# Performance work log

Hardware: AMD Instinct MI355X
Metric: run time of the kernel (lower is better)

## Reference

```python
import jax, jax.numpy as jnp
import numpy as np
import math

DIM = 1024

def setup_inputs() -> dict:
    key = jax.random.key(0)
    ks = jax.random.split(key, 5)
    X = jax.random.normal(ks[0], (4, 2048, DIM), dtype=jnp.float32)
    # Linear params (stored as [in, out] so y = x @ W + b)
    W_in = jax.random.normal(ks[1], (DIM, 3 * DIM), dtype=jnp.float32) / math.sqrt(DIM)
    b_in = jnp.zeros((3 * DIM,), dtype=jnp.float32)
    W_out = jax.random.normal(ks[2], (DIM, DIM), dtype=jnp.float32) / math.sqrt(DIM)
    b_out = jnp.zeros((DIM,), dtype=jnp.float32)
    return {"X": X, "W_in": W_in, "b_in": b_in, "W_out": W_out, "b_out": b_out}

def reference(X, W_in, b_in, W_out, b_out):
    dim = X.shape[-1]
    QKV = X @ W_in + b_in                       # [B, S, 3*dim]
    Q, K, V = jnp.split(QKV, 3, axis=-1)        # each [B, S, dim]
    scores = jnp.einsum('bqd,bkd->bqk', Q, K) / math.sqrt(dim)  # [B, S, S]
    attn = jax.nn.softmax(scores, axis=-1)
    out = jnp.einsum('bqk,bkd->bqd', attn, V)   # [B, S, dim]
    return out @ W_out + b_out
```

## Files before the change

kernel.cpp:

```cpp
#include <hip/hip_runtime.h>
#include <hip/hip_bf16.h>
#include <math.h>

typedef __attribute__((ext_vector_type(8))) __bf16 bf16x8;
typedef __attribute__((ext_vector_type(4))) float f32x4;
typedef __attribute__((ext_vector_type(4))) unsigned int u32x4;

#define DIM 1024
#define SEQ 2048
#define BATCH 4
#define ROWS (BATCH*SEQ)

#define BAR() do { asm volatile("" ::: "memory"); __builtin_amdgcn_s_barrier(); asm volatile("" ::: "memory"); } while(0)
#define WAITV(n) asm volatile("s_waitcnt vmcnt(" #n ")" ::: "memory")
#define WAITL(n) asm volatile("s_waitcnt lgkmcnt(" #n ")" ::: "memory")
#define SCHED0() __builtin_amdgcn_sched_barrier(0)
#define PRIO(x) __builtin_amdgcn_s_setprio(x)

#define DSR(d, a, off) do { u32x4 _t; \
  asm volatile("ds_read_b128 %0, %1 offset:" #off : "=v"(_t) : "v"(a)); \
  (d) = __builtin_bit_cast(bf16x8, _t); } while(0)

__device__ __forceinline__ unsigned short f2bf(float f) {
  unsigned int u = __float_as_uint(f);
  u += 0x7FFF + ((u >> 16) & 1);
  return (unsigned short)(u >> 16);
}
__device__ __forceinline__ unsigned short to_bf_bits(float v) { return f2bf(v); }
__device__ __forceinline__ unsigned short to_bf_bits(unsigned short v) { return v; }

__device__ __forceinline__ void gload_lds16(const void* g, void* lds) {
  __builtin_amdgcn_global_load_lds((__attribute__((address_space(1))) void*)g,
                                   (__attribute__((address_space(3))) void*)lds,
                                   16, 0, 0);
}

__global__ __launch_bounds__(256)
void conv_f32_bf16(const float* __restrict__ src, unsigned short* __restrict__ dst, int n8) {
  int i = blockIdx.x * blockDim.x + threadIdx.x;
  if (i >= n8) return;
  const float4* s = reinterpret_cast<const float4*>(src) + (size_t)i * 2;
  float4 a = s[0], b = s[1];
  union { unsigned short h[8]; uint4 v; } p;
  p.h[0]=f2bf(a.x); p.h[1]=f2bf(a.y); p.h[2]=f2bf(a.z); p.h[3]=f2bf(a.w);
  p.h[4]=f2bf(b.x); p.h[5]=f2bf(b.y); p.h[6]=f2bf(b.z); p.h[7]=f2bf(b.w);
  reinterpret_cast<uint4*>(dst)[i] = p.v;
}

template<typename Tin>
__global__ __launch_bounds__(1024)
void transpose_conv(const Tin* __restrict__ src, int ldsrc, size_t sstride,
                    unsigned short* __restrict__ dst, int lddst, size_t dstride) {
  __shared__ unsigned short tile[32][33];
  const Tin* s = src + (size_t)blockIdx.z * sstride;
  unsigned short* d = dst + (size_t)blockIdx.z * dstride;
  int tx = threadIdx.x, ty = threadIdx.y;
  int r = blockIdx.y * 32 + ty, c = blockIdx.x * 32 + tx;
  tile[ty][tx] = to_bf_bits(s[(size_t)r * ldsrc + c]);
  __syncthreads();
  d[(size_t)(blockIdx.x * 32 + ty) * lddst + blockIdx.y * 32 + tx] = tile[tx][ty];
}

#define EPI_QKV 0
#define EPI_F32 1
#define EPI_BF16 2
#define EPI_BIAS_F32 3

template<int BN, int EPI>
__global__ __launch_bounds__(512, 2)
void gemm8(const unsigned short* __restrict__ A, int lda, size_t sA,
           const unsigned short* __restrict__ B, int ldb, size_t sB,
           void* __restrict__ C, int ldc, size_t sC,
           const float* __restrict__ bias, int K) {
  constexpr int NREP = BN / 64;
  constexpr int NW = 16 * NREP;
  __shared__ unsigned short As[2 * 256 * 64];
  __shared__ unsigned short Bs[2 * BN * 64];

  const int tid = threadIdx.x;
  const int lane = tid & 63, wave = tid >> 6;
  const int wm = wave >> 2, wn = wave & 3;
  const int fr = lane & 15, fk = lane >> 4;
  const int tileM = blockIdx.y * 256, tileN = blockIdx.x * BN;
  const unsigned short* Ab = A + (size_t)blockIdx.z * sA;
  const unsigned short* Bb = B + (size_t)blockIdx.z * sB;

  const int srow = tid >> 3;
  const int sg = (tid & 7) ^ (srow & 7);

  auto stageA = [&](int buf, int half, int k0) {
#pragma unroll
    for (int q = 0; q < 2; ++q) {
      int rl = half * 128 + q * 64 + srow;
      gload_lds16(Ab + (size_t)(tileM + rl) * lda + k0 + sg * 8,
                  &As[buf * (256 * 64) + rl * 64 + (tid & 7) * 8]);
    }
  };
  auto stageB = [&](int buf, int half, int k0) {
#pragma unroll
    for (int q = 0; q < 2; ++q) {
      int rl = half * 128 + q * 64 + srow;
      gload_lds16(Bb + (size_t)(tileN + rl) * ldb + k0 + sg * 8,
                  &Bs[buf * (BN * 64) + rl * 64 + (tid & 7) * 8]);
    }
  };

  f32x4 acc[8][NREP];
#pragma unroll
  for (int m = 0; m < 8; ++m)
#pragma unroll
    for (int n = 0; n < NREP; ++n) acc[m][n] = (f32x4){0.f, 0.f, 0.f, 0.f};

  const int NS = K >> 6;
  const unsigned asb = (unsigned)(size_t)(__attribute__((address_space(3))) unsigned short*)As;
  const unsigned bsb = (unsigned)(size_t)(__attribute__((address_space(3))) unsigned short*)Bs;
  const unsigned aoff = (unsigned)((wm * 128 + fr) * 128 + ((fk ^ (fr & 7)) << 4));
  const unsigned boff = (unsigned)((wn * NW + fr) * 128 + ((fk ^ (fr & 7)) << 4));
  auto aBase = [&](int b) { return asb + (unsigned)b * 32768u + aoff; };
  auto bBase = [&](int b) { return bsb + (unsigned)b * (unsigned)(BN * 128) + boff; };

  if constexpr (BN == 256) {
    bf16x8 afLo[4][2], afHi[4][2], bgA[2][2], bgB[2][2];
    stageB(0, 0, 0); stageB(0, 1, 0); stageA(0, 0, 0); stageA(0, 1, 0);
    if (NS > 1) { stageB(1, 0, 64); stageB(1, 1, 64); WAITV(4); } else { WAITV(0); }
    BAR();
    {
      unsigned a0 = aBase(0), a1 = a0 ^ 64u, b0 = bBase(0), b1 = b0 ^ 64u;
      DSR(afLo[0][0], a0, 0); DSR(afLo[1][0], a0, 2048); DSR(afLo[2][0], a0, 4096); DSR(afLo[3][0], a0, 6144);
      DSR(afLo[0][1], a1, 0); DSR(afLo[1][1], a1, 2048); DSR(afLo[2][1], a1, 4096); DSR(afLo[3][1], a1, 6144);
      DSR(bgA[0][0], b0, 0); DSR(bgA[1][0], b0, 2048);
      DSR(bgA[0][1], b1, 0); DSR(bgA[1][1], b1, 2048);
    }
    for (int t = 0; t < NS; ++t) {
      const int cb = t & 1, nb = cb ^ 1;
      const unsigned cA0 = aBase(cb), cA1 = cA0 ^ 64u, cB0 = bBase(cb), cB1 = cB0 ^ 64u;
      const unsigned nA0 = aBase(nb), nA1 = nA0 ^ 64u, nB0 = bBase(nb), nB1 = nB0 ^ 64u;
      const int k1 = (t + 1) << 6, k2 = (t + 2) << 6;
      DSR(bgB[0][0], cB0, 4096); DSR(bgB[1][0], cB0, 6144);
      DSR(bgB[0][1], cB1, 4096); DSR(bgB[1][1], cB1, 6144);
      if (t + 1 < NS) stageA(nb, 0, k1);
      BAR(); WAITL(4); SCHED0();
      PRIO(1);
#pragma unroll
      for (int kk = 0; kk < 2; ++kk)
#pragma unroll
        for (int m = 0; m < 4; ++m)
#pragma unroll
          for (int n = 0; n < 2; ++n)
            acc[m][n] = __builtin_amdgcn_mfma_f32_16x16x32_bf16(afLo[m][kk], bgA[n][kk], acc[m][n], 0, 0, 0);
      PRIO(0); SCHED0();
      BAR();
      DSR(afHi[0][0], cA0, 8192); DSR(afHi[1][0], cA0, 10240); DSR(afHi[2][0], cA0, 12288); DSR(afHi[3][0], cA0, 14336);
      DSR(afHi[0][1], cA1, 8192); DSR(afHi[1][1], cA1, 10240); DSR(afHi[2][1], cA1, 12288); DSR(afHi[3][1], cA1, 14336);
      if (t + 1 < NS) stageA(nb, 1, k1);
      if (t + 2 < NS) stageB(cb, 0, k2);
      BAR(); WAITL(8); SCHED0();
      PRIO(1);
#pragma unroll
      for (int kk = 0; kk < 2; ++kk)
#pragma unroll
        for (int m = 0; m < 4; ++m)
#pragma unroll
          for (int n = 0; n < 2; ++n)
            acc[m][2 + n] = __builtin_amdgcn_mfma_f32_16x16x32_bf16(afLo[m][kk], bgB[n][kk], acc[m][2 + n], 0, 0, 0);
      PRIO(0); SCHED0();
      BAR();
      if (t + 2 < NS) stageB(cb, 1, k2);
      BAR(); WAITL(0); SCHED0();
      PRIO(1);
#pragma unroll
      for (int kk = 0; kk < 2; ++kk)
#pragma unroll
        for (int m = 0; m < 4; ++m)
#pragma unroll
          for (int n = 0; n < 2; ++n)
            acc[4 + m][n] = __builtin_amdgcn_mfma_f32_16x16x32_bf16(afHi[m][kk], bgA[n][kk], acc[4 + m][n], 0, 0, 0);
      PRIO(0); SCHED0();
      if (t + 1 < NS) { if (t + 2 < NS) { WAITV(4); } else { WAITV(0); } }
      BAR();
      if (t + 1 < NS) {
        DSR(afLo[0][0], nA0, 0); DSR(afLo[1][0], nA0, 2048); DSR(afLo[2][0], nA0, 4096); DSR(afLo[3][0], nA0, 6144);
        DSR(afLo[0][1], nA1, 0); DSR(afLo[1][1], nA1, 2048); DSR(afLo[2][1], nA1, 4096); DSR(afLo[3][1], nA1, 6144);
        DSR(bgA[0][0], nB0, 0); DSR(bgA[1][0], nB0, 2048);
        DSR(bgA[0][1], nB1, 0); DSR(bgA[1][1], nB1, 2048);
      }
      SCHED0();
      PRIO(1);
#pragma unroll
      for (int kk = 0; kk < 2; ++kk)
#pragma unroll
        for (int m = 0; m < 4; ++m)
#pragma unroll
          for (int n = 0; n < 2; ++n)
            acc[4 + m][2 + n] = __builtin_amdgcn_mfma_f32_16x16x32_bf16(afHi[m][kk], bgB[n][kk], acc[4 + m][2 + n], 0, 0, 0);
      PRIO(0); SCHED0();
      BAR();
    }
  } else {
    bf16x8 a0f[4], a1f[4], h0f[4], h1f[4], b0f[2], b1f[2];
    stageB(0, 0, 0); stageA(0, 0, 0); stageA(0, 1, 0);
    if (NS > 1) { stageB(1, 0, 64); WAITV(2); } else { WAITV(0); }
    BAR();
    {
      unsigned a0 = aBase(0), b0 = bBase(0);
      DSR(a0f[0], a0, 0); DSR(a0f[1], a0, 2048); DSR(a0f[2], a0, 4096); DSR(a0f[3], a0, 6144);
      DSR(b0f[0], b0, 0); DSR(b0f[1], b0, 2048);
    }
    for (int t = 0; t < NS; ++t) {
      const int cb = t & 1, nb = cb ^ 1;
      const unsigned cA0 = aBase(cb), cA1 = cA0 ^ 64u, cB0 = bBase(cb), cB1 = cB0 ^ 64u;
      const unsigned nA0 = aBase(nb), nB0 = bBase(nb);
      const int k1 = (t + 1) << 6, k2 = (t + 2) << 6;
      DSR(a1f[0], cA1, 0); DSR(a1f[1], cA1, 2048); DSR(a1f[2], cA1, 4096); DSR(a1f[3], cA1, 6144);
      DSR(b1f[0], cB1, 0); DSR(b1f[1], cB1, 2048);
      if (t + 1 < NS) stageA(nb, 0, k1);
      BAR(); WAITL(6); SCHED0();
      PRIO(1);
#pragma unroll
      for (int m = 0; m < 4; ++m)
#pragma unroll
        for (int n = 0; n < 2; ++n)
          acc[m][n] = __builtin_amdgcn_mfma_f32_16x16x32_bf16(a0f[m], b0f[n], acc[m][n], 0, 0, 0);
      PRIO(0); SCHED0();
      BAR();
      DSR(h0f[0], cA0, 8192); DSR(h0f[1], cA0, 10240); DSR(h0f[2], cA0, 12288); DSR(h0f[3], cA0, 14336);
      if (t + 1 < NS) stageA(nb, 1, k1);
      BAR(); WAITL(4); SCHED0();
      PRIO(1);
#pragma unroll
      for (int m = 0; m < 4; ++m)
#pragma unroll
        for (int n = 0; n < 2; ++n)
          acc[m][n] = __builtin_amdgcn_mfma_f32_16x16x32_bf16(a1f[m], b1f[n], acc[m][n], 0, 0, 0);
      PRIO(0); SCHED0();
      BAR();
      DSR(h1f[0], cA1, 8192); DSR(h1f[1], cA1, 10240); DSR(h1f[2], cA1, 12288); DSR(h1f[3], cA1, 14336);
      if (t + 2 < NS) stageB(cb, 0, k2);
      BAR(); WAITL(4); SCHED0();
      PRIO(1);
#pragma unroll
      for (int m = 0; m < 4; ++m)
#pragma unroll
        for (int n = 0; n < 2; ++n)
          acc[4 + m][n] = __builtin_amdgcn_mfma_f32_16x16x32_bf16(h0f[m], b0f[n], acc[4 + m][n], 0, 0, 0);
      PRIO(0); SCHED0();
      if (t + 1 < NS) { if (t + 2 < NS) { WAITV(2); } else { WAITV(0); } }
      BAR();
      if (t + 1 < NS) {
        DSR(a0f[0], nA0, 0); DSR(a0f[1], nA0, 2048); DSR(a0f[2], nA0, 4096); DSR(a0f[3], nA0, 6144);
        DSR(b0f[0], nB0, 0); DSR(b0f[1], nB0, 2048);
        WAITL(6);
      } else {
        WAITL(0);
      }
      SCHED0();
      PRIO(1);
#pragma unroll
      for (int m = 0; m < 4; ++m)
#pragma unroll
        for (int n = 0; n < 2; ++n)
          acc[4 + m][n] = __builtin_amdgcn_mfma_f32_16x16x32_bf16(h1f[m], b1f[n], acc[4 + m][n], 0, 0, 0);
      PRIO(0); SCHED0();
      BAR();
    }
  }

#pragma unroll
  for (int m = 0; m < 8; ++m)
#pragma unroll
    for (int n = 0; n < NREP; ++n)
#pragma unroll
      for (int j = 0; j < 4; ++j) {
        int row = tileM + wm * 128 + m * 16 + fk * 4 + j;
        int col = tileN + wn * NW + n * 16 + fr;
        float v = acc[m][n][j];
        if (EPI == EPI_QKV) {
          v += bias[col];
          if (col < DIM) v *= 0.03125f;
          ((unsigned short*)C + (size_t)blockIdx.z * sC)[(size_t)row * ldc + col] = f2bf(v);
        } else if (EPI == EPI_BF16) {
          ((unsigned short*)C + (size_t)blockIdx.z * sC)[(size_t)row * ldc + col] = f2bf(v);
        } else if (EPI == EPI_BIAS_F32) {
          ((float*)C + (size_t)blockIdx.z * sC)[(size_t)row * ldc + col] = v + bias[col];
        } else {
          ((float*)C + (size_t)blockIdx.z * sC)[(size_t)row * ldc + col] = v;
        }
      }
}

__global__ __launch_bounds__(256)
void softmax_kernel(float* __restrict__ S, size_t zstride) {
  __shared__ float red[8];
  float* row = S + (size_t)blockIdx.y * zstride + (size_t)blockIdx.x * SEQ;
  const int tid = threadIdx.x;
  const int lane = tid & 63, wave = tid >> 6;
  const float4* src = reinterpret_cast<const float4*>(row) + tid * 2;
  float4 a = src[0], b = src[1];
  float v[8] = {a.x, a.y, a.z, a.w, b.x, b.y, b.z, b.w};
  float m = v[0];
#pragma unroll
  for (int i = 1; i < 8; ++i) m = fmaxf(m, v[i]);
  for (int o = 32; o; o >>= 1) m = fmaxf(m, __shfl_xor(m, o));
  if (lane == 0) red[wave] = m;
  __syncthreads();
  m = fmaxf(fmaxf(red[0], red[1]), fmaxf(red[2], red[3]));
  float e[8], s = 0.f;
#pragma unroll
  for (int i = 0; i < 8; ++i) { e[i] = expf(v[i] - m); s += e[i]; }
  for (int o = 32; o; o >>= 1) s += __shfl_xor(s, o);
  if (lane == 0) red[4 + wave] = s;
  __syncthreads();
  s = red[4] + red[5] + red[6] + red[7];
  float inv = 1.f / s;
  union { unsigned short h[8]; uint4 u; } p;
#pragma unroll
  for (int i = 0; i < 8; ++i) p.h[i] = f2bf(e[i] * inv);
  reinterpret_cast<uint4*>(row)[tid] = p.u;
}

extern "C" void kernel_launch(void* const* d_in, const int* in_sizes, int n_in,
                              void* d_out, int out_size, void* d_ws, size_t ws_size,
                              hipStream_t stream) {
  const float* X     = (const float*)d_in[0];
  const float* W_in  = (const float*)d_in[1];
  const float* b_in  = (const float*)d_in[2];
  const float* W_out = (const float*)d_in[3];
  const float* b_out = (const float*)d_in[4];
  float* out = (float*)d_out;
  char* ws = (char*)d_ws;

  size_t o = 0;
  auto alloc = [&](size_t bytes) { size_t r = o; o += (bytes + 255) & ~(size_t)255; return r; };
  unsigned short* Xbf   = (unsigned short*)(ws + alloc((size_t)ROWS * DIM * 2));
  unsigned short* WinT  = (unsigned short*)(ws + alloc((size_t)3 * DIM * DIM * 2));
  unsigned short* WoutT = (unsigned short*)(ws + alloc((size_t)DIM * DIM * 2));
  unsigned short* QKV   = (unsigned short*)(ws + alloc((size_t)ROWS * 3 * DIM * 2));
  size_t fixed = o;
  size_t per_batch = (((size_t)SEQ * SEQ * 4 + 255) & ~(size_t)255) +
                     (((size_t)DIM * SEQ * 2 + 255) & ~(size_t)255);
  int G = (ws_size >= fixed + 4 * per_batch) ? BATCH : 1;
  float*          Sc = (float*)(ws + alloc((size_t)G * SEQ * SEQ * 4));
  unsigned short* Vt = (unsigned short*)(ws + alloc((size_t)G * DIM * SEQ * 2));
  unsigned short* O  = Xbf;

  conv_f32_bf16<<<(ROWS * DIM / 8 + 255) / 256, 256, 0, stream>>>(X, Xbf, ROWS * DIM / 8);
  transpose_conv<float><<<dim3(3 * DIM / 32, DIM / 32, 1), dim3(32, 32), 0, stream>>>(
      W_in, 3 * DIM, 0, WinT, DIM, 0);
  transpose_conv<float><<<dim3(DIM / 32, DIM / 32, 1), dim3(32, 32), 0, stream>>>(
      W_out, DIM, 0, WoutT, DIM, 0);
  gemm8<128, EPI_QKV><<<dim3(3 * DIM / 128, ROWS / 256, 1), 512, 0, stream>>>(
      Xbf, DIM, 0, WinT, DIM, 0, QKV, 3 * DIM, 0, b_in, DIM);

  for (int b0 = 0; b0 < BATCH; b0 += G) {
    const unsigned short* Qb = QKV + (size_t)b0 * SEQ * 3 * DIM;
    const unsigned short* Kb = Qb + DIM;
    const unsigned short* Vb = Qb + 2 * DIM;
    transpose_conv<unsigned short><<<dim3(DIM / 32, SEQ / 32, G), dim3(32, 32), 0, stream>>>(
        Vb, 3 * DIM, (size_t)SEQ * 3 * DIM, Vt, SEQ, (size_t)DIM * SEQ);
    gemm8<256, EPI_F32><<<dim3(SEQ / 256, SEQ / 256, G), 512, 0, stream>>>(
        Qb, 3 * DIM, (size_t)SEQ * 3 * DIM, Kb, 3 * DIM, (size_t)SEQ * 3 * DIM,
        Sc, SEQ, (size_t)SEQ * SEQ, nullptr, DIM);
    softmax_kernel<<<dim3(SEQ, G), 256, 0, stream>>>(Sc, (size_t)SEQ * SEQ);
    gemm8<128, EPI_BF16><<<dim3(DIM / 128, SEQ / 256, G), 512, 0, stream>>>(
        (const unsigned short*)Sc, 2 * SEQ, (size_t)2 * SEQ * SEQ,
        Vt, SEQ, (size_t)DIM * SEQ,
        O + (size_t)b0 * SEQ * DIM, DIM, (size_t)SEQ * DIM, nullptr, SEQ);
  }
  gemm8<128, EPI_BIAS_F32><<<dim3(DIM / 128, ROWS / 256, 1), 512, 0, stream>>>(
      O, DIM, 0, WoutT, DIM, 0, out, DIM, 0, b_out, DIM);
}
```

Before: 228.5 us.

## Fuse softmax into PV GEMM and add triple-buffered BN128 GEMM kernel

Removes the separate softmax pass. A new pv_fused kernel computes row max and sum with an online reduction over the fp32 scores. It then exponentiates, normalizes and converts score tiles to bf16 while staging them into LDS for the P·V MFMA loop, with a 3-deep ring buffer for V. The QKV and output projections move to a new gemm1b kernel with a simpler triple-buffered pipeline. The fused kernel reads the fp32 score matrix twice (stats pass plus operand pass) and recomputes exp inside the GEMM, in exchange for dropping the softmax write and reread.

```diff
diff --git a/kernel.cpp b/kernel.cpp
--- a/kernel.cpp
+++ b/kernel.cpp
@@ -20,6 +20,8 @@
 #define DSR(d, a, off) do { u32x4 _t; \
   asm volatile("ds_read_b128 %0, %1 offset:" #off : "=v"(_t) : "v"(a)); \
   (d) = __builtin_bit_cast(bf16x8, _t); } while(0)
+#define GLD4(d, p, off) asm volatile("global_load_dwordx4 %0, %1, off offset:" #off \
+  : "=&v"(d) : "v"(p))
 
 __device__ __forceinline__ unsigned short f2bf(float f) {
   unsigned int u = __float_as_uint(f);
@@ -66,17 +68,15 @@
 #define EPI_BF16 2
 #define EPI_BIAS_F32 3
 
-template<int BN, int EPI>
+template<int EPI>
 __global__ __launch_bounds__(512, 2)
 void gemm8(const unsigned short* __restrict__ A, int lda, size_t sA,
            const unsigned short* __restrict__ B, int ldb, size_t sB,
            void* __restrict__ C, int ldc, size_t sC,
            const float* __restrict__ bias, int K) {
-  constexpr int NREP = BN / 64;
-  constexpr int NW = 16 * NREP;
+  constexpr int BN = 256, NREP = 4, NW = 64;
   __shared__ unsigned short As[2 * 256 * 64];
   __shared__ unsigned short Bs[2 * BN * 64];
-
   const int tid = threadIdx.x;
   const int lane = tid & 63, wave = tid >> 6;
   const int wm = wave >> 2, wn = wave & 3;
@@ -84,7 +84,6 @@
   const int tileM = blockIdx.y * 256, tileN = blockIdx.x * BN;
   const unsigned short* Ab = A + (size_t)blockIdx.z * sA;
   const unsigned short* Bb = B + (size_t)blockIdx.z * sB;
-
   const int srow = tid >> 3;
   const int sg = (tid & 7) ^ (srow & 7);
 
@@ -119,150 +118,81 @@
   auto aBase = [&](int b) { return asb + (unsigned)b * 32768u + aoff; };
   auto bBase = [&](int b) { return bsb + (unsigned)b * (unsigned)(BN * 128) + boff; };
 
-  if constexpr (BN == 256) {
-    bf16x8 afLo[4][2], afHi[4][2], bgA[2][2], bgB[2][2];
-    stageB(0, 0, 0); stageB(0, 1, 0); stageA(0, 0, 0); stageA(0, 1, 0);
-    if (NS > 1) { stageB(1, 0, 64); stageB(1, 1, 64); WAITV(4); } else { WAITV(0); }
+  bf16x8 afLo[4][2], afHi[4][2], bgA[2][2], bgB[2][2];
+  stageB(0, 0, 0); stageB(0, 1, 0); stageA(0, 0, 0); stageA(0, 1, 0);
+  if (NS > 1) { stageB(1, 0, 64); stageB(1, 1, 64); WAITV(4); } else { WAITV(0); }
+  BAR();
+  {
+    unsigned a0 = aBase(0), a1 = a0 ^ 64u, b0 = bBase(0), b1 = b0 ^ 64u;
+    DSR(afLo[0][0], a0, 0); DSR(afLo[1][0], a0, 2048); DSR(afLo[2][0], a0, 4096); DSR(afLo[3][0], a0, 6144);
+    DSR(afLo[0][1], a1, 0); DSR(afLo[1][1], a1, 2048); DSR(afLo[2][1], a1, 4096); DSR(afLo[3][1], a1, 6144);
+    DSR(bgA[0][0], b0, 0); DSR(bgA[1][0], b0, 2048);
+    DSR(bgA[0][1], b1, 0); DSR(bgA[1][1], b1, 2048);
+  }
+  for (int t = 0; t < NS; ++t) {
+    const int cb = t & 1, nb = cb ^ 1;
+    const unsigned cA0 = aBase(cb), cA1 = cA0 ^ 64u, cB0 = bBase(cb), cB1 = cB0 ^ 64u;
+    const unsigned nA0 = aBase(nb), nA1 = nA0 ^ 64u, nB0 = bBase(nb), nB1 = nB0 ^ 64u;
+    const int k1 = (t + 1) << 6, k2 = (t + 2) << 6;
+    DSR(bgB[0][0], cB0, 4096); DSR(bgB[1][0], cB0, 6144);
+    DSR(bgB[0][1], cB1, 4096); DSR(bgB[1][1], cB1, 6144);
+    if (t + 1 < NS) stageA(nb, 0, k1);
+    BAR(); WAITL(4); SCHED0();
+    PRIO(1);
+#pragma unroll
+    for (int kk = 0; kk < 2; ++kk)
+#pragma unroll
+      for (int m = 0; m < 4; ++m)
+#pragma unroll
+        for (int n = 0; n < 2; ++n)
+          acc[m][n] = __builtin_amdgcn_mfma_f32_16x16x32_bf16(afLo[m][kk], bgA[n][kk], acc[m][n], 0, 0, 0);
+    PRIO(0); SCHED0();
     BAR();
-    {
-      unsigned a0 = aBase(0), a1 = a0 ^ 64u, b0 = bBase(0), b1 = b0 ^ 64u;
-      DSR(afLo[0][0], a0, 0); DSR(afLo[1][0], a0, 2048); DSR(afLo[2][0], a0, 4096); DSR(afLo[3][0], a0, 6144);
-      DSR(afLo[0][1], a1, 0); DSR(afLo[1][1], a1, 2048); DSR(afLo[2][1], a1, 4096); DSR(afLo[3][1], a1, 6144);
-      DSR(bgA[0][0], b0, 0); DSR(bgA[1][0], b0, 2048);
-      DSR(bgA[0][1], b1, 0); DSR(bgA[1][1], b1, 2048);
-    }
-    for (int t = 0; t < NS; ++t) {
-      const int cb = t & 1, nb = cb ^ 1;
-      const unsigned cA0 = aBase(cb), cA1 = cA0 ^ 64u, cB0 = bBase(cb), cB1 = cB0 ^ 64u;
-      const unsigned nA0 = aBase(nb), nA1 = nA0 ^ 64u, nB0 = bBase(nb), nB1 = nB0 ^ 64u;
-      const int k1 = (t + 1) << 6, k2 = (t + 2) << 6;
-      DSR(bgB[0][0], cB0, 4096); DSR(bgB[1][0], cB0, 6144);
-      DSR(bgB[0][1], cB1, 4096); DSR(bgB[1][1], cB1, 6144);
-      if (t + 1 < NS) stageA(nb, 0, k1);
-      BAR(); WAITL(4); SCHED0();
-      PRIO(1);
-#pragma unroll
-      for (int kk = 0; kk < 2; ++kk)
-#pragma unroll
-        for (int m = 0; m < 4; ++m)
-#pragma unroll
-          for (int n = 0; n < 2; ++n)
-            acc[m][n] = __builtin_amdgcn_mfma_f32_16x16x32_bf16(afLo[m][kk], bgA[n][kk], acc[m][n], 0, 0, 0);
-      PRIO(0); SCHED0();
-      BAR();
-      DSR(afHi[0][0], cA0, 8192); DSR(afHi[1][0], cA0, 10240); DSR(afHi[2][0], cA0, 12288); DSR(afHi[3][0], cA0, 14336);
-      DSR(afHi[0][1], cA1, 8192); DSR(afHi[1][1], cA1, 10240); DSR(afHi[2][1], cA1, 12288); DSR(afHi[3][1], cA1, 14336);
-      if (t + 1 < NS) stageA(nb, 1, k1);
-      if (t + 2 < NS) stageB(cb, 0, k2);
-      BAR(); WAITL(8); SCHED0();
-      PRIO(1);
-#pragma unroll
-      for (int kk = 0; kk < 2; ++kk)
-#pragma unroll
-        for (int m = 0; m < 4; ++m)
-#pragma unroll
-          for (int n = 0; n < 2; ++n)
-            acc[m][2 + n] = __builtin_amdgcn_mfma_f32_16x16x32_bf16(afLo[m][kk], bgB[n][kk], acc[m][2 + n], 0, 0, 0);
-      PRIO(0); SCHED0();
-      BAR();
-      if (t + 2 < NS) stageB(cb, 1, k2);
-      BAR(); WAITL(0); SCHED0();
-      PRIO(1);
-#pragma unroll
-      for (int kk = 0; kk < 2; ++kk)
-#pragma unroll
-        for (int m = 0; m < 4; ++m)
-#pragma unroll
-          for (int n = 0; n < 2; ++n)
-            acc[4 + m][n] = __builtin_amdgcn_mfma_f32_16x16x32_bf16(afHi[m][kk], bgA[n][kk], acc[4 + m][n], 0, 0, 0);
-      PRIO(0); SCHED0();
-      if (t + 1 < NS) { if (t + 2 < NS) { WAITV(4); } else { WAITV(0); } }
-      BAR();
-      if (t + 1 < NS) {
-        DSR(afLo[0][0], nA0, 0); DSR(afLo[1][0], nA0, 2048); DSR(afLo[2][0], nA0, 4096); DSR(afLo[3][0], nA0, 6144);
-        DSR(afLo[0][1], nA1, 0); DSR(afLo[1][1], nA1, 2048); DSR(afLo[2][1], nA1, 4096); DSR(afLo[3][1], nA1, 6144);
-        DSR(bgA[0][0], nB0, 0); DSR(bgA[1][0], nB0, 2048);
-        DSR(bgA[0][1], nB1, 0); DSR(bgA[1][1], nB1, 2048);
-      }
-      SCHED0();
-      PRIO(1);
-#pragma unroll
-      for (int kk = 0; kk < 2; ++kk)
-#pragma unroll
-        for (int m = 0; m < 4; ++m)
-#pragma unroll
-          for (int n = 0; n < 2; ++n)
-            acc[4 + m][2 + n] = __builtin_amdgcn_mfma_f32_16x16x32_bf16(afHi[m][kk], bgB[n][kk], acc[4 + m][2 + n], 0, 0, 0);
-      PRIO(0); SCHED0();
-      BAR();
-    }
-  } else {
-    bf16x8 a0f[4], a1f[4], h0f[4], h1f[4], b0f[2], b1f[2];
-    stageB(0, 0, 0); stageA(0, 0, 0); stageA(0, 1, 0);
-    if (NS > 1) { stageB(1, 0, 64); WAITV(2); } else { WAITV(0); }
+    DSR(afHi[0][0], cA0, 8192); DSR(afHi[1][0], cA0, 10240); DSR(afHi[2][0], cA0, 12288); DSR(afHi[3][0], cA0, 14336);
+    DSR(afHi[0][1], cA1, 8192); DSR(afHi[1][1], cA1, 10240); DSR(afHi[2][1], cA1, 12288); DSR(afHi[3][1], cA1, 14336);
+    if (t + 1 < NS) stageA(nb, 1, k1);
+    if (t + 2 < NS) stageB(cb, 0, k2);
+    BAR(); WAITL(8); SCHED0();
+    PRIO(1);
+#pragma unroll
+    for (int kk = 0; kk < 2; ++kk)
+#pragma unroll
+      for (int m = 0; m < 4; ++m)
+#pragma unroll
+        for (int n = 0; n < 2; ++n)
+          acc[m][2 + n] = __builtin_amdgcn_mfma_f32_16x16x32_bf16(afLo[m][kk], bgB[n][kk], acc[m][2 + n], 0, 0, 0);
+    PRIO(0); SCHED0();
     BAR();
-    {
-      unsigned a0 = aBase(0), b0 = bBase(0);
-      DSR(a0f[0], a0, 0); DSR(a0f[1], a0, 2048); DSR(a0f[2], a0, 4096); DSR(a0f[3], a0, 6144);
-      DSR(b0f[0], b0, 0); DSR(b0f[1], b0, 2048);
-    }
-    for (int t = 0; t < NS; ++t) {
-      const int cb = t & 1, nb = cb ^ 1;
-      const unsigned cA0 = aBase(cb), cA1 = cA0 ^ 64u, cB0 = bBase(cb), cB1 = cB0 ^ 64u;
-      const unsigned nA0 = aBase(nb), nB0 = bBase(nb);
-      const int k1 = (t + 1) << 6, k2 = (t + 2) << 6;
-      DSR(a1f[0], cA1, 0); DSR(a1f[1], cA1, 2048); DSR(a1f[2], cA1, 4096); DSR(a1f[3], cA1, 6144);
-      DSR(b1f[0], cB1, 0); DSR(b1f[1], cB1, 2048);
-      if (t + 1 < NS) stageA(nb, 0, k1);
-      BAR(); WAITL(6); SCHED0();
-      PRIO(1);
-#pragma unroll
-      for (int m = 0; m < 4; ++m)
-#pragma unroll
-        for (int n = 0; n < 2; ++n)
-          acc[m][n] = __builtin_amdgcn_mfma_f32_16x16x32_bf16(a0f[m], b0f[n], acc[m][n], 0, 0, 0);
-      PRIO(0); SCHED0();
-      BAR();
-      DSR(h0f[0], cA0, 8192); DSR(h0f[1], cA0, 10240); DSR(h0f[2], cA0, 12288); DSR(h0f[3], cA0, 14336);
-      if (t + 1 < NS) stageA(nb, 1, k1);
-      BAR(); WAITL(4); SCHED0();
-      PRIO(1);
-#pragma unroll
-      for (int m = 0; m < 4; ++m)
-#pragma unroll
-        for (int n = 0; n < 2; ++n)
-          acc[m][n] = __builtin_amdgcn_mfma_f32_16x16x32_bf16(a1f[m], b1f[n], acc[m][n], 0, 0, 0);
-      PRIO(0); SCHED0();
-      BAR();
-      DSR(h1f[0], cA1, 8192); DSR(h1f[1], cA1, 10240); DSR(h1f[2], cA1, 12288); DSR(h1f[3], cA1, 14336);
-      if (t + 2 < NS) stageB(cb, 0, k2);
-      BAR(); WAITL(4); SCHED0();
-      PRIO(1);
-#pragma unroll
-      for (int m = 0; m < 4; ++m)
-#pragma unroll
-        for (int n = 0; n < 2; ++n)
-          acc[4 + m][n] = __builtin_amdgcn_mfma_f32_16x16x32_bf16(h0f[m], b0f[n], acc[4 + m][n], 0, 0, 0);
-      PRIO(0); SCHED0();
-      if (t + 1 < NS) { if (t + 2 < NS) { WAITV(2); } else { WAITV(0); } }
-      BAR();
-      if (t + 1 < NS) {
-        DSR(a0f[0], nA0, 0); DSR(a0f[1], nA0, 2048); DSR(a0f[2], nA0, 4096); DSR(a0f[3], nA0, 6144);
-        DSR(b0f[0], nB0, 0); DSR(b0f[1], nB0, 2048);
-        WAITL(6);
-      } else {
-        WAITL(0);
-      }
-      SCHED0();
-      PRIO(1);
-#pragma unroll
-      for (int m = 0; m < 4; ++m)
-#pragma unroll
-        for (int n = 0; n < 2; ++n)
-          acc[4 + m][n] = __builtin_amdgcn_mfma_f32_16x16x32_bf16(h1f[m], b1f[n], acc[4 + m][n], 0, 0, 0);
-      PRIO(0); SCHED0();
-      BAR();
-    }
+    if (t + 2 < NS) stageB(cb, 1, k2);
+    BAR(); WAITL(0); SCHED0();
+    PRIO(1);
+#pragma unroll
+    for (int kk = 0; kk < 2; ++kk)
+#pragma unroll
+      for (int m = 0; m < 4; ++m)
+#pragma unroll
+        for (int n = 0; n < 2; ++n)
+          acc[4 + m][n] = __builtin_amdgcn_mfma_f32_16x16x32_bf16(afHi[m][kk], bgA[n][kk], acc[4 + m][n], 0, 0, 0);
+    PRIO(0); SCHED0();
+    if (t + 1 < NS) { if (t + 2 < NS) { WAITV(4); } else { WAITV(0); } }
+    BAR();
+    if (t + 1 < NS) {
+      DSR(afLo[0][0], nA0, 0); DSR(afLo[1][0], nA0, 2048); DSR(afLo[2][0], nA0, 4096); DSR(afLo[3][0], nA0, 6144);
+      DSR(afLo[0][1], nA1, 0); DSR(afLo[1][1], nA1, 2048); DSR(afLo[2][1], nA1, 4096); DSR(afLo[3][1], nA1, 6144);
+      DSR(bgA[0][0], nB0, 0); DSR(bgA[1][0], nB0, 2048);
+      DSR(bgA[0][1], nB1, 0); DSR(bgA[1][1], nB1, 2048);
+    }
+    SCHED0();
+    PRIO(1);
+#pragma unroll
+    for (int kk = 0; kk < 2; ++kk)
+#pragma unroll
+      for (int m = 0; m < 4; ++m)
+#pragma unroll
+        for (int n = 0; n < 2; ++n)
+          acc[4 + m][2 + n] = __builtin_amdgcn_mfma_f32_16x16x32_bf16(afHi[m][kk], bgB[n][kk], acc[4 + m][2 + n], 0, 0, 0);
+    PRIO(0); SCHED0();
+    BAR();
   }
 
 #pragma unroll
@@ -274,48 +204,257 @@
         int row = tileM + wm * 128 + m * 16 + fk * 4 + j;
         int col = tileN + wn * NW + n * 16 + fr;
         float v = acc[m][n][j];
+        if (EPI == EPI_F32) {
+          ((float*)C + (size_t)blockIdx.z * sC)[(size_t)row * ldc + col] = v;
+        } else {
+          ((float*)C + (size_t)blockIdx.z * sC)[(size_t)row * ldc + col] = v + bias[col];
+        }
+      }
+}
+
+template<int EPI>
+__global__ __launch_bounds__(512, 2)
+void gemm1b(const unsigned short* __restrict__ A, int lda,
+            const unsigned short* __restrict__ B, int ldb,
+            void* __restrict__ C, int ldc,
+            const float* __restrict__ bias, int K) {
+  __shared__ unsigned short As[3 * 256 * 64];
+  __shared__ unsigned short Bs[3 * 128 * 64];
+  const int tid = threadIdx.x;
+  const int lane = tid & 63, wave = tid >> 6;
+  const int wm = wave >> 2, wn = wave & 3;
+  const int fr = lane & 15, fk = lane >> 4;
+  const int tileM = blockIdx.y * 256, tileN = blockIdx.x * 128;
+  const int srow = tid >> 3;
+
+  auto stageT = [&](int ring, int k0) {
+#pragma unroll
+    for (int q = 0; q < 4; ++q) {
+      int rl = q * 64 + srow;
+      int sg = (tid & 7) ^ (rl & 7);
+      gload_lds16(A + (size_t)(tileM + rl) * lda + k0 + sg * 8,
+                  &As[ring * (256 * 64) + rl * 64 + (tid & 7) * 8]);
+    }
+#pragma unroll
+    for (int q = 0; q < 2; ++q) {
+      int rl = q * 64 + srow;
+      int sg = (tid & 7) ^ (rl & 7);
+      gload_lds16(B + (size_t)(tileN + rl) * ldb + k0 + sg * 8,
+                  &Bs[ring * (128 * 64) + rl * 64 + (tid & 7) * 8]);
+    }
+  };
+
+  f32x4 acc[8][2];
+#pragma unroll
+  for (int m = 0; m < 8; ++m)
+#pragma unroll
+    for (int n = 0; n < 2; ++n) acc[m][n] = (f32x4){0.f, 0.f, 0.f, 0.f};
+
+  const int NS = K >> 6;
+  const unsigned asb = (unsigned)(size_t)(__attribute__((address_space(3))) unsigned short*)As;
+  const unsigned bsb = (unsigned)(size_t)(__attribute__((address_space(3))) unsigned short*)Bs;
+  const unsigned aoff = (unsigned)((wm * 128 + fr) * 128 + ((fk ^ (fr & 7)) << 4));
+  const unsigned boff = (unsigned)((wn * 32 + fr) * 128 + ((fk ^ (fr & 7)) << 4));
+
+  stageT(0, 0); stageT(1, 64);
+  WAITV(6); BAR();
+
+  bf16x8 afLo[4][2], afHi[4][2], bg[2][2];
+  int ring = 0;
+  for (int t = 0; t < NS; ++t) {
+    const unsigned aT0 = asb + (unsigned)ring * 32768u + aoff, aT1 = aT0 ^ 64u;
+    const unsigned bT0 = bsb + (unsigned)ring * 16384u + boff, bT1 = bT0 ^ 64u;
+    if (t + 2 < NS) stageT((t + 2) % 3, (t + 2) << 6);
+    DSR(afLo[0][0], aT0, 0); DSR(afLo[1][0], aT0, 2048); DSR(afLo[2][0], aT0, 4096); DSR(afLo[3][0], aT0, 6144);
+    DSR(afLo[0][1], aT1, 0); DSR(afLo[1][1], aT1, 2048); DSR(afLo[2][1], aT1, 4096); DSR(afLo[3][1], aT1, 6144);
+    DSR(bg[0][0], bT0, 0); DSR(bg[1][0], bT0, 2048);
+    DSR(bg[0][1], bT1, 0); DSR(bg[1][1], bT1, 2048);
+    WAITL(0); SCHED0();
+    PRIO(1);
+#pragma unroll
+    for (int kk = 0; kk < 2; ++kk)
+#pragma unroll
+      for (int m = 0; m < 4; ++m)
+#pragma unroll
+        for (int n = 0; n < 2; ++n)
+          acc[m][n] = __builtin_amdgcn_mfma_f32_16x16x32_bf16(afLo[m][kk], bg[n][kk], acc[m][n], 0, 0, 0);
+    PRIO(0); SCHED0();
+    DSR(afHi[0][0], aT0, 8192); DSR(afHi[1][0], aT0, 10240); DSR(afHi[2][0], aT0, 12288); DSR(afHi[3][0], aT0, 14336);
+    DSR(afHi[0][1], aT1, 8192); DSR(afHi[1][1], aT1, 10240); DSR(afHi[2][1], aT1, 12288); DSR(afHi[3][1], aT1, 14336);
+    WAITL(0); SCHED0();
+    PRIO(1);
+#pragma unroll
+    for (int kk = 0; kk < 2; ++kk)
+#pragma unroll
+      for (int m = 0; m < 4; ++m)
+#pragma unroll
+        for (int n = 0; n < 2; ++n)
+          acc[4 + m][n] = __builtin_amdgcn_mfma_f32_16x16x32_bf16(afHi[m][kk], bg[n][kk], acc[4 + m][n], 0, 0, 0);
+    PRIO(0); SCHED0();
+    if (t + 1 < NS) { if (t + 2 < NS) { WAITV(6); } else { WAITV(0); } }
+    BAR();
+    ring = (ring + 1) % 3;
+  }
+
+#pragma unroll
+  for (int m = 0; m < 8; ++m)
+#pragma unroll
+    for (int n = 0; n < 2; ++n)
+#pragma unroll
+      for (int j = 0; j < 4; ++j) {
+        int row = tileM + wm * 128 + m * 16 + fk * 4 + j;
+        int col = tileN + wn * 32 + n * 16 + fr;
+        float v = acc[m][n][j];
         if (EPI == EPI_QKV) {
           v += bias[col];
           if (col < DIM) v *= 0.03125f;
-          ((unsigned short*)C + (size_t)blockIdx.z * sC)[(size_t)row * ldc + col] = f2bf(v);
-        } else if (EPI == EPI_BF16) {
-          ((unsigned short*)C + (size_t)blockIdx.z * sC)[(size_t)row * ldc + col] = f2bf(v);
+          ((unsigned short*)C)[(size_t)row * ldc + col] = f2bf(v);
         } else if (EPI == EPI_BIAS_F32) {
-          ((float*)C + (size_t)blockIdx.z * sC)[(size_t)row * ldc + col] = v + bias[col];
+          ((float*)C)[(size_t)row * ldc + col] = v + bias[col];
         } else {
-          ((float*)C + (size_t)blockIdx.z * sC)[(size_t)row * ldc + col] = v;
+          ((unsigned short*)C)[(size_t)row * ldc + col] = f2bf(v);
         }
       }
 }
 
-__global__ __launch_bounds__(256)
-void softmax_kernel(float* __restrict__ S, size_t zstride) {
-  __shared__ float red[8];
-  float* row = S + (size_t)blockIdx.y * zstride + (size_t)blockIdx.x * SEQ;
+__global__ __launch_bounds__(512, 2)
+void pv_fused(const float* __restrict__ S, size_t sS,
+              const unsigned short* __restrict__ Vt, size_t sV,
+              unsigned short* __restrict__ O, size_t sO) {
+  __shared__ unsigned short As[2 * 128 * 64];
+  __shared__ unsigned short Bs[3 * 256 * 64];
+  __shared__ float mrow[128], ilrow[128];
   const int tid = threadIdx.x;
   const int lane = tid & 63, wave = tid >> 6;
-  const float4* src = reinterpret_cast<const float4*>(row) + tid * 2;
-  float4 a = src[0], b = src[1];
-  float v[8] = {a.x, a.y, a.z, a.w, b.x, b.y, b.z, b.w};
-  float m = v[0];
-#pragma unroll
-  for (int i = 1; i < 8; ++i) m = fmaxf(m, v[i]);
-  for (int o = 32; o; o >>= 1) m = fmaxf(m, __shfl_xor(m, o));
-  if (lane == 0) red[wave] = m;
+  const int wm = wave >> 2, wn = wave & 3;
+  const int fr = lane & 15, fk = lane >> 4;
+  const int tileM = blockIdx.y * 128, tileN = blockIdx.x * 256;
+  const float* Sb = S + (size_t)blockIdx.z * sS;
+  const unsigned short* Vb = Vt + (size_t)blockIdx.z * sV;
+
+  {
+    int r = tid >> 2, q = tid & 3;
+    const float4* rowp = (const float4*)(Sb + (size_t)(tileM + r) * SEQ);
+    float m = -3.4e38f, l = 0.f;
+    for (int i = q; i < SEQ / 4; i += 4) {
+      float4 v = rowp[i];
+      float mx = fmaxf(fmaxf(v.x, v.y), fmaxf(v.z, v.w));
+      if (mx > m) { l *= __expf(m - mx); m = mx; }
+      l += __expf(v.x - m) + __expf(v.y - m) + __expf(v.z - m) + __expf(v.w - m);
+    }
+#pragma unroll
+    for (int o = 1; o < 4; o <<= 1) {
+      float mo = __shfl_xor(m, o), lo = __shfl_xor(l, o);
+      float mn = fmaxf(m, mo);
+      l = l * __expf(m - mn) + lo * __expf(mo - mn); m = mn;
+    }
+    if (q == 0) { mrow[r] = m; ilrow[r] = 1.f / l; }
+  }
   __syncthreads();
-  m = fmaxf(fmaxf(red[0], red[1]), fmaxf(red[2], red[3]));
-  float e[8], s = 0.f;
-#pragma unroll
-  for (int i = 0; i < 8; ++i) { e[i] = expf(v[i] - m); s += e[i]; }
-  for (int o = 32; o; o >>= 1) s += __shfl_xor(s, o);
-  if (lane == 0) red[4 + wave] = s;
-  __syncthreads();
-  s = red[4] + red[5] + red[6] + red[7];
-  float inv = 1.f / s;
-  union { unsigned short h[8]; uint4 u; } p;
-#pragma unroll
-  for (int i = 0; i < 8; ++i) p.h[i] = f2bf(e[i] * inv);
-  reinterpret_cast<uint4*>(row)[tid] = p.u;
+
+  const int sr = tid >> 2;
+  const float mr = mrow[sr], ilr = ilrow[sr];
+  const int scol = (tid & 3) * 16;
+  const int s0 = (tid & 3) * 2;
+  const int p0 = s0 ^ (sr & 7), p1 = (s0 + 1) ^ (sr & 7);
+  const int srow = tid >> 3;
+
+  auto stageB = [&](int ring, int k0) {
+#pragma unroll
+    for (int q = 0; q < 4; ++q) {
+      int rl = q * 64 + srow;
+      int sg = (tid & 7) ^ (rl & 7);
+      gload_lds16(Vb + (size_t)(tileN + rl) * SEQ + k0 + sg * 8,
+                  &Bs[ring * (256 * 64) + rl * 64 + (tid & 7) * 8]);
+    }
+  };
+  float4 st0, st1, st2, st3;
+  auto issueA = [&](int k0) {
+    const float* ap = Sb + (size_t)(tileM + sr) * SEQ + k0 + scol;
+    GLD4(st0, ap, 0); GLD4(st1, ap, 16); GLD4(st2, ap, 32); GLD4(st3, ap, 48);
+  };
+  auto writeA = [&](int buf) {
+    union { unsigned short h[8]; uint4 u; } a, b;
+    a.h[0]=f2bf(__expf(st0.x-mr)*ilr); a.h[1]=f2bf(__expf(st0.y-mr)*ilr);
+    a.h[2]=f2bf(__expf(st0.z-mr)*ilr); a.h[3]=f2bf(__expf(st0.w-mr)*ilr);
+    a.h[4]=f2bf(__expf(st1.x-mr)*ilr); a.h[5]=f2bf(__expf(st1.y-mr)*ilr);
+    a.h[6]=f2bf(__expf(st1.z-mr)*ilr); a.h[7]=f2bf(__expf(st1.w-mr)*ilr);
+    b.h[0]=f2bf(__expf(st2.x-mr)*ilr); b.h[1]=f2bf(__expf(st2.y-mr)*ilr);
+    b.h[2]=f2bf(__expf(st2.z-mr)*ilr); b.h[3]=f2bf(__expf(st2.w-mr)*ilr);
+    b.h[4]=f2bf(__expf(st3.x-mr)*ilr); b.h[5]=f2bf(__expf(st3.y-mr)*ilr);
+    b.h[6]=f2bf(__expf(st3.z-mr)*ilr); b.h[7]=f2bf(__expf(st3.w-mr)*ilr);
+    *(uint4*)&As[buf * (128 * 64) + sr * 64 + p0 * 8] = a.u;
+    *(uint4*)&As[buf * (128 * 64) + sr * 64 + p1 * 8] = b.u;
+  };
+
+  f32x4 acc[4][4];
+#pragma unroll
+  for (int m = 0; m < 4; ++m)
+#pragma unroll
+    for (int n = 0; n < 4; ++n) acc[m][n] = (f32x4){0.f, 0.f, 0.f, 0.f};
+
+  const int NS = SEQ >> 6;
+  const unsigned asb = (unsigned)(size_t)(__attribute__((address_space(3))) unsigned short*)As;
+  const unsigned bsb = (unsigned)(size_t)(__attribute__((address_space(3))) unsigned short*)Bs;
+  const unsigned aoff = (unsigned)((wm * 64 + fr) * 128 + ((fk ^ (fr & 7)) << 4));
+  const unsigned boff = (unsigned)((wn * 64 + fr) * 128 + ((fk ^ (fr & 7)) << 4));
+
+  issueA(0);
+  stageB(0, 0); stageB(1, 64);
+  WAITV(8); SCHED0();
+  writeA(0);
+  WAITV(4);
+  WAITL(0); BAR();
+
+  bf16x8 af[4][2], bgA[2][2], bgB[2][2];
+  for (int t = 0; t < NS; ++t) {
+    const int cb = t & 1, nb = cb ^ 1;
+    const unsigned aT0 = asb + (unsigned)cb * 16384u + aoff, aT1 = aT0 ^ 64u;
+    const unsigned bT0 = bsb + (unsigned)(t % 3) * 32768u + boff, bT1 = bT0 ^ 64u;
+    if (t + 1 < NS) issueA((t + 1) << 6);
+    if (t + 2 < NS) stageB((t + 2) % 3, (t + 2) << 6);
+    DSR(af[0][0], aT0, 0); DSR(af[1][0], aT0, 2048); DSR(af[2][0], aT0, 4096); DSR(af[3][0], aT0, 6144);
+    DSR(af[0][1], aT1, 0); DSR(af[1][1], aT1, 2048); DSR(af[2][1], aT1, 4096); DSR(af[3][1], aT1, 6144);
+    DSR(bgA[0][0], bT0, 0); DSR(bgA[1][0], bT0, 2048);
+    DSR(bgA[0][1], bT1, 0); DSR(bgA[1][1], bT1, 2048);
+    WAITL(0); SCHED0();
+    PRIO(1);
+#pragma unroll
+    for (int kk = 0; kk < 2; ++kk)
+#pragma unroll
+      for (int m = 0; m < 4; ++m)
+#pragma unroll
+        for (int n = 0; n < 2; ++n)
+          acc[m][n] = __builtin_amdgcn_mfma_f32_16x16x32_bf16(af[m][kk], bgA[n][kk], acc[m][n], 0, 0, 0);
+    PRIO(0); SCHED0();
+    DSR(bgB[0][0], bT0, 4096); DSR(bgB[1][0], bT0, 6144);
+    DSR(bgB[0][1], bT1, 4096); DSR(bgB[1][1], bT1, 6144);
+    if (t + 2 < NS) { WAITV(4); } else { WAITV(0); }
+    SCHED0();
+    if (t + 1 < NS) writeA(nb);
+    WAITL(0); SCHED0();
+    PRIO(1);
+#pragma unroll
+    for (int kk = 0; kk < 2; ++kk)
+#pragma unroll
+      for (int m = 0; m < 4; ++m)
+#pragma unroll
+        for (int n = 0; n < 2; ++n)
+          acc[m][2 + n] = __builtin_amdgcn_mfma_f32_16x16x32_bf16(af[m][kk], bgB[n][kk], acc[m][2 + n], 0, 0, 0);
+    PRIO(0); SCHED0();
+    BAR();
+  }
+
+#pragma unroll
+  for (int m = 0; m < 4; ++m)
+#pragma unroll
+    for (int n = 0; n < 4; ++n)
+#pragma unroll
+      for (int j = 0; j < 4; ++j) {
+        int row = tileM + wm * 64 + m * 16 + fk * 4 + j;
+        int col = tileN + wn * 64 + n * 16 + fr;
+        (O + (size_t)blockIdx.z * sO)[(size_t)row * DIM + col] = f2bf(acc[m][n][j]);
+      }
 }
 
 extern "C" void kernel_launch(void* const* d_in, const int* in_sizes, int n_in,
@@ -341,15 +480,15 @@
   int G = (ws_size >= fixed + 4 * per_batch) ? BATCH : 1;
   float*          Sc = (float*)(ws + alloc((size_t)G * SEQ * SEQ * 4));
   unsigned short* Vt = (unsigned short*)(ws + alloc((size_t)G * DIM * SEQ * 2));
-  unsigned short* O  = Xbf;
+  unsigned short* Ob = Xbf;
 
   conv_f32_bf16<<<(ROWS * DIM / 8 + 255) / 256, 256, 0, stream>>>(X, Xbf, ROWS * DIM / 8);
   transpose_conv<float><<<dim3(3 * DIM / 32, DIM / 32, 1), dim3(32, 32), 0, stream>>>(
       W_in, 3 * DIM, 0, WinT, DIM, 0);
   transpose_conv<float><<<dim3(DIM / 32, DIM / 32, 1), dim3(32, 32), 0, stream>>>(
       W_out, DIM, 0, WoutT, DIM, 0);
-  gemm8<128, EPI_QKV><<<dim3(3 * DIM / 128, ROWS / 256, 1), 512, 0, stream>>>(
-      Xbf, DIM, 0, WinT, DIM, 0, QKV, 3 * DIM, 0, b_in, DIM);
+  gemm1b<EPI_QKV><<<dim3(3 * DIM / 128, ROWS / 256, 1), 512, 0, stream>>>(
+      Xbf, DIM, WinT, DIM, QKV, 3 * DIM, b_in, DIM);
 
   for (int b0 = 0; b0 < BATCH; b0 += G) {
     const unsigned short* Qb = QKV + (size_t)b0 * SEQ * 3 * DIM;
@@ -357,15 +496,13 @@
     const unsigned short* Vb = Qb + 2 * DIM;
     transpose_conv<unsigned short><<<dim3(DIM / 32, SEQ / 32, G), dim3(32, 32), 0, stream>>>(
         Vb, 3 * DIM, (size_t)SEQ * 3 * DIM, Vt, SEQ, (size_t)DIM * SEQ);
-    gemm8<256, EPI_F32><<<dim3(SEQ / 256, SEQ / 256, G), 512, 0, stream>>>(
+    gemm8<EPI_F32><<<dim3(SEQ / 256, SEQ / 256, G), 512, 0, stream>>>(
         Qb, 3 * DIM, (size_t)SEQ * 3 * DIM, Kb, 3 * DIM, (size_t)SEQ * 3 * DIM,
         Sc, SEQ, (size_t)SEQ * SEQ, nullptr, DIM);
-    softmax_kernel<<<dim3(SEQ, G), 256, 0, stream>>>(Sc, (size_t)SEQ * SEQ);
-    gemm8<128, EPI_BF16><<<dim3(DIM / 128, SEQ / 256, G), 512, 0, stream>>>(
-        (const unsigned short*)Sc, 2 * SEQ, (size_t)2 * SEQ * SEQ,
-        Vt, SEQ, (size_t)DIM * SEQ,
-        O + (size_t)b0 * SEQ * DIM, DIM, (size_t)SEQ * DIM, nullptr, SEQ);
+    pv_fused<<<dim3(DIM / 256, SEQ / 128, G), 512, 0, stream>>>(
+        Sc, (size_t)SEQ * SEQ, Vt, (size_t)DIM * SEQ,
+        Ob + (size_t)b0 * SEQ * DIM, (size_t)SEQ * DIM);
   }
-  gemm8<128, EPI_BIAS_F32><<<dim3(DIM / 128, ROWS / 256, 1), 512, 0, stream>>>(
-      O, DIM, 0, WoutT, DIM, 0, out, DIM, 0, b_out, DIM);
-}
+  gemm1b<EPI_BIAS_F32><<<dim3(DIM / 128, ROWS / 256, 1), 512, 0, stream>>>(
+      Ob, DIM, WoutT, DIM, out, DIM, b_out, DIM);
+}
```

After: 300.1 us. 1.31x slower.
